# Kernel optimization log

Measured on AMD Instinct MI355X. Metric: run time of the kernel, lower is better.

The kernel has to match this reference:

```python
import jax, jax.numpy as jnp
import numpy as np

D, P, MC = 512, 256, 128   # state dim, obs dim, control dim
H, M, T = 32, 64, 1024     # num filters, Hankel/filter length, horizon
GAMMA = 0.9


def setup_inputs() -> dict:
    rng = np.random.default_rng(0)
    # Stable dynamics: scale spectral radius to 0.95
    A = rng.standard_normal((D, D)).astype(np.float32)
    A *= np.float32(0.95 / np.max(np.abs(np.linalg.eigvals(A))))
    B = (rng.standard_normal((D, MC)) / np.sqrt(D)).astype(np.float32)
    C = (rng.standard_normal((P, D)) / np.sqrt(D)).astype(np.float32)
    # SPD cost matrices
    Q_obs = np.eye(P, dtype=np.float32)
    R = (0.1 * np.eye(MC)).astype(np.float32)
    # LQR-like feedback gain (small, applied to y_obs as in the source)
    K = (0.02 * rng.standard_normal((MC, P))).astype(np.float32)
    # Spectral filters from Hankel matrix: Z_ij = gamma^(i+j+2) * 2/((i+j+2)^3-(i+j+2))
    idx = np.arange(M)
    ij = idx[:, None] + idx[None, :] + 2
    Z = (GAMMA ** ij) * 2.0 / (ij ** 3 - ij)
    w, V = np.linalg.eigh(Z)
    sigma = np.abs(w[-H:])
    phi = V[:, -H:]
    sigma_phi = (sigma ** 0.25)[:, None] * phi.T        # [H, M]
    sigma_phi_M = sigma_phi.astype(np.float32)
    # sum over the inner l-loop of sigma_phi_m (the source sums contributions over l)
    s_m = sigma_phi.sum(axis=1).astype(np.float32)       # [H]
    # Learned controller tensor M_il -> [m_control, H, h, p]
    M_tensor = (0.01 * rng.standard_normal((MC, H, H, P))).astype(np.float32)
    x0 = rng.standard_normal(D).astype(np.float32)
    return {
        "A": jnp.asarray(A), "B": jnp.asarray(B), "C": jnp.asarray(C),
        "Q_obs": jnp.asarray(Q_obs), "R": jnp.asarray(R), "K": jnp.asarray(K),
        "M_tensor": jnp.asarray(M_tensor),
        "sigma_phi_M": jnp.asarray(sigma_phi_M), "s_m": jnp.asarray(s_m),
        "x0": jnp.asarray(x0),
    }


def reference(A, B, C, Q_obs, R, K, M_tensor, sigma_phi_M, s_m, x0):
    h, m = sigma_phi_M.shape          # filters, history window
    mc = B.shape[1]
    p = C.shape[0]

    # CAB[i] = C @ A^i @ B for i = 0..h  (Markov parameters for y_nat)
    def pow_step(Ap, _):
        return Ap @ A, C @ (Ap @ B)
    _, CAB = jax.lax.scan(pow_step, jnp.eye(A.shape[0], dtype=A.dtype), None, length=h + 1)  # [h+1, p, mc]

    # Pre-contract M_tensor with the inner filter weights (sum over j/l):
    # u_pert[c] = sum_{i,k,p'} M2[c,i,p'] * sigma_phi_M[i,k] * y_nat_{t-k}[p']
    M2 = jnp.einsum('cijq,j->ciq', M_tensor, s_m)  # [mc, h, p]

    def step(carry, _):
        x, u_buf, y_buf = carry            # x:[d], u_buf:[h+1,mc] newest-first, y_buf:[m,p] newest-first
        y_obs = C @ x                      # [p]
        # natural observation: strip effect of past controls
        y_nat = y_obs - jnp.einsum('ipc,ic->p', CAB, u_buf)
        y_buf = jnp.concatenate([y_nat[None, :], y_buf[:-1]], axis=0)
        # spectral projection of y_nat history, then contract with learned tensor
        y_proj = sigma_phi_M @ y_buf       # [h, p]
        u_pert = jnp.einsum('ciq,iq->c', M2, y_proj)  # [mc]
        u = -(K @ y_obs) + u_pert
        cost = y_obs @ (Q_obs @ y_obs) + u @ (R @ u)
        u_buf = jnp.concatenate([u[None, :], u_buf[:-1]], axis=0)
        x = A @ x + B @ u
        return (x, u_buf, y_buf), cost

    init = (x0,
            jnp.zeros((h + 1, mc), dtype=x0.dtype),
            jnp.zeros((m, p), dtype=x0.dtype))
    _, costs = jax.lax.scan(step, init, None, length=T)
    return costs  # [T] per-step losses
```

## Files before the change

kernel.cpp:

```cpp
#include <hip/hip_runtime.h>

#define TPB 256
#define MAXJ 48

#define SC_N 128
#define YD0 128
#define YU0 144
#define WD0 151
#define WU0 159
#define DT0 166
#define XP0 182
#define XR0 214
#define U0 230
#define NWG 238
#define NGRP 8
#define GCH 30

__device__ __forceinline__ void cst(float* p, float v) {
  __hip_atomic_store(p, v, __ATOMIC_RELAXED, __HIP_MEMORY_SCOPE_AGENT);
}
__device__ __forceinline__ void cstu(unsigned* p, unsigned v) {
  __hip_atomic_store(p, v, __ATOMIC_RELAXED, __HIP_MEMORY_SCOPE_AGENT);
}
__device__ __forceinline__ unsigned cldu(const unsigned* p) {
  return __hip_atomic_load(p, __ATOMIC_RELAXED, __HIP_MEMORY_SCOPE_AGENT);
}
__device__ __forceinline__ float cld(const float* p) {
  return __hip_atomic_load(p, __ATOMIC_RELAXED, __HIP_MEMORY_SCOPE_AGENT);
}
__device__ __forceinline__ float2 cld2(const float* p) {
  unsigned long long u = __hip_atomic_load(
      reinterpret_cast<const unsigned long long*>(p), __ATOMIC_RELAXED,
      __HIP_MEMORY_SCOPE_AGENT);
  float2 v;
  __builtin_memcpy(&v, &u, 8);
  return v;
}

__device__ __forceinline__ void grid_barrier(unsigned* __restrict__ arr,
                                             unsigned* __restrict__ grp,
                                             int bid, int tid, unsigned phase) {
  asm volatile("s_waitcnt vmcnt(0)" ::: "memory");
  __syncthreads();
  if (tid == 0) cstu(arr + (bid << 5), phase);
  if (bid < NGRP) {
    const int lo = bid * GCH;
    const int n = (NWG - lo < GCH) ? (NWG - lo) : GCH;
    if (tid < n) {
      while (cldu(arr + ((lo + tid) << 5)) < phase) __builtin_amdgcn_s_sleep(1);
    }
    __syncthreads();
    if (tid == 0) cstu(grp + (bid << 5), phase);
  }
  if (tid < NGRP) {
    while (cldu(grp + (tid << 5)) < phase) __builtin_amdgcn_s_sleep(1);
  }
  __atomic_signal_fence(__ATOMIC_SEQ_CST);
  __syncthreads();
}

__device__ void gemm_tile(const float* __restrict__ X, const float* __restrict__ Y,
                          float* __restrict__ Z, int M, int N, int Kd,
                          int mtile, int ntile) {
  __shared__ float Xs[16][65];
  __shared__ float Ys[16][65];
  const int tx = threadIdx.x & 15;
  const int ty = threadIdx.x >> 4;
  const int mbase = mtile * 64;
  const int nbase = ntile * 64;
  float acc[4][4] = {};
  for (int k0 = 0; k0 < Kd; k0 += 16) {
#pragma unroll
    for (int r = 0; r < 4; ++r) {
      int idx = threadIdx.x + 256 * r;
      int mm = idx >> 4, kk = idx & 15;
      int gm = mbase + mm, gk = k0 + kk;
      Xs[kk][mm] = (gm < M && gk < Kd) ? X[(size_t)gm * Kd + gk] : 0.f;
      int nn = idx & 63, k2 = idx >> 6;
      int gn = nbase + nn, gk2 = k0 + k2;
      Ys[k2][nn] = (gk2 < Kd && gn < N) ? Y[(size_t)gk2 * N + gn] : 0.f;
    }
    __syncthreads();
#pragma unroll
    for (int kk = 0; kk < 16; ++kk) {
      float xv[4], yv[4];
#pragma unroll
      for (int a = 0; a < 4; ++a) xv[a] = Xs[kk][ty * 4 + a];
#pragma unroll
      for (int b = 0; b < 4; ++b) yv[b] = Ys[kk][tx * 4 + b];
#pragma unroll
      for (int a = 0; a < 4; ++a)
#pragma unroll
        for (int b = 0; b < 4; ++b) acc[a][b] += xv[a] * yv[b];
    }
    __syncthreads();
  }
#pragma unroll
  for (int a = 0; a < 4; ++a) {
    int gm = mbase + ty * 4 + a;
    if (gm < M) {
#pragma unroll
      for (int b = 0; b < 4; ++b) {
        int gn = nbase + tx * 4 + b;
        if (gn < N) Z[(size_t)gm * N + gn] = acc[a][b];
      }
    }
  }
}

struct JobBatch {
  int n;
  int start[MAXJ + 1];
  int xsel[MAXJ], xoff[MAXJ], ysel[MAXJ], yoff[MAXJ], zoff[MAXJ];
  int M[MAXJ], N[MAXJ], K[MAXJ];
};

__global__ __launch_bounds__(256) void multi_gemm(JobBatch jb,
    const float* __restrict__ A, const float* __restrict__ Bm,
    const float* __restrict__ C, const float* __restrict__ Km,
    float* __restrict__ ws) {
  int b = blockIdx.x;
  int j = 0;
  while (j < jb.n - 1 && b >= jb.start[j + 1]) ++j;
  int rel = b - jb.start[j];
  const float* bases[5] = {ws, A, Bm, C, Km};
  const float* X = bases[jb.xsel[j]] + jb.xoff[j];
  const float* Y = bases[jb.ysel[j]] + jb.yoff[j];
  float* Z = ws + jb.zoff[j];
  int tn = jb.N[j] >> 6;
  gemm_tile(X, Y, Z, jb.M[j], jb.N[j], jb.K[j], rel / tn, rel % tn);
}

__global__ __launch_bounds__(256) void m2_kernel(const float* __restrict__ MT,
    const float* __restrict__ sm, float* __restrict__ M2g) {
  int idx = blockIdx.x * 256 + threadIdx.x;
  if (idx >= 128 * 32 * 256) return;
  int q = idx & 255;
  int ci = idx >> 8;
  const float* base = MT + (size_t)ci * 32 * 256 + q;
  float acc = 0.f;
#pragma unroll
  for (int j = 0; j < 32; ++j) acc += base[j * 256] * sm[j];
  M2g[idx] = acc;
}

__global__ __launch_bounds__(256) void wfir_kernel(const float* __restrict__ M2g,
    const float* __restrict__ Phi, float* __restrict__ W) {
  int idx = blockIdx.x * 256 + threadIdx.x;
  if (idx >= 64 * 32768) return;
  int j = idx >> 15;
  int cq = idx & 32767;
  int c = cq >> 8;
  int q = cq & 255;
  float acc = 0.f;
#pragma unroll
  for (int i = 0; i < 32; ++i)
    acc = fmaf(Phi[(i << 6) | j], M2g[(size_t)(((c << 5) | i) << 8) | q], acc);
  W[idx] = acc;
}

__global__ __launch_bounds__(256) void axpy_acl(const float* __restrict__ A,
    const float* __restrict__ BKC, float* __restrict__ Acl, float* __restrict__ P1) {
  int i = blockIdx.x * 256 + threadIdx.x;
  if (i < 262144) {
    float v = A[i] - BKC[i];
    Acl[i] = v;
    P1[i] = v;
  }
}

__global__ void init_kernel(const float* __restrict__ x0, float* __restrict__ xh,
    float* __restrict__ eh, float* __restrict__ ynh, float* __restrict__ uh0,
    float* __restrict__ dbnd, unsigned* __restrict__ arr,
    unsigned* __restrict__ grp) {
  int i = blockIdx.x * 256 + threadIdx.x;
  int stride = gridDim.x * 256;
  for (int k = i; k < 524288; k += stride) cst(xh + k, 0.f);
  for (int k = i; k < 139264; k += stride) cst(eh + k, 0.f);
  for (int k = i; k < 262144; k += stride) cst(ynh + k, 0.f);
  for (int k = i; k < 8192; k += stride) cst(uh0 + k, 0.f);
  for (int k = i; k < NWG * 32; k += stride) cstu(arr + k, 0u);
  for (int k = i; k < NGRP * 32; k += stride) cstu(grp + k, 0u);
  if (i < 512) cst(dbnd + i, x0[i]);
}

__global__ __launch_bounds__(TPB, 1) void main_kernel(
    const float* __restrict__ B, const float* __restrict__ C,
    const float* __restrict__ x0, const float* __restrict__ Wfir,
    const float* __restrict__ KC, const float* __restrict__ W0C,
    const float* __restrict__ Pp, const float* __restrict__ CAp,
    const float* __restrict__ W0CAp, const float* __restrict__ Rnp,
    const float* __restrict__ AB33p, const float* __restrict__ CAB33p,
    const float* __restrict__ W0CAB33p, const float* __restrict__ A8k,
    float* __restrict__ xh, float* __restrict__ uh0, float* __restrict__ eh,
    float* __restrict__ ynh, float* __restrict__ dbnd,
    unsigned* __restrict__ arr, unsigned* __restrict__ grp) {
  __shared__ float smA[64 * 256];
  __shared__ float smY[8 * 256];
  __shared__ float smV[512];
  __shared__ float smW[8 * 128];
  __shared__ float smVx[8 * 516];
  __shared__ float redsc[4][16];
  const int bid = blockIdx.x;
  const int tid = threadIdx.x;

  if (bid < SC_N) {
    for (int i = tid; i < 16384; i += TPB) {
      int j = i >> 8;
      smA[i] = (j >= 1) ? Wfir[(size_t)j * 32768 + bid * 256 + (i & 255)] : 0.f;
    }
  }
  __syncthreads();

#pragma unroll 1
  for (int ph = 0; ph <= 130; ++ph) {
    const int T = ph * 8;

    if (bid < SC_N) {
      if (ph >= 1 && ph < 129) {
        const int Ty = T - 8;
        const int c = bid;
        for (int i2 = tid; i2 < 1024; i2 += TPB) {
          float2 v = cld2(ynh + (size_t)Ty * 256 + 2 * i2);
          smY[2 * i2] = v.x;
          smY[2 * i2 + 1] = v.y;
        }
        __syncthreads();
        const int q = tid;
        float yreg[8];
#pragma unroll
        for (int s = 0; s < 8; ++s) yreg[s] = smY[s * 256 + q];
        const int wv = tid >> 6;
        const int lane = tid & 63;
#pragma unroll
        for (int kt = 0; kt < 5; ++kt) {
          const int r0 = 1 + 16 * kt;
          float wreg[23];
#pragma unroll
          for (int i = 0; i < 23; ++i) {
            const int j = r0 - 7 + i;
            wreg[i] = (j >= 1 && j <= 63) ? smA[j * 256 + q] : 0.f;
          }
          float acc[16];
#pragma unroll
          for (int a = 0; a < 16; ++a) acc[a] = 0.f;
#pragma unroll
          for (int a = 0; a < 16; ++a)
#pragma unroll
            for (int s = 0; s < 8; ++s) acc[a] += wreg[a + 7 - s] * yreg[s];
#pragma unroll
          for (int a = 0; a < 16; ++a) {
            float v = acc[a];
            v += __shfl_xor(v, 32);
            v += __shfl_xor(v, 16);
            v += __shfl_xor(v, 8);
            v += __shfl_xor(v, 4);
            v += __shfl_xor(v, 2);
            v += __shfl_xor(v, 1);
            if (lane == 0) redsc[wv][a] = v;
          }
          __syncthreads();
          if (tid < 16) {
            const int r = r0 + tid;
            if (r <= 70) {
              float sum = redsc[0][tid] + redsc[1][tid] + redsc[2][tid] + redsc[3][tid];
              atomicAdd(&eh[(size_t)(Ty + r) * 128 + c], sum);
            }
          }
          __syncthreads();
        }
      }
    } else if (bid < YU0) {
      if (ph < 128) {
        const int r = bid - YD0;
        const int s = r >> 1;
        const int half = (r & 1) << 7;
        {
          float2 v = cld2(dbnd + (size_t)ph * 512 + 2 * tid);
          smV[2 * tid] = v.x;
          smV[2 * tid + 1] = v.y;
        }
        __syncthreads();
        const float* Mrow = (s == 0) ? C : (CAp + (size_t)(s - 1) * 131072);
        const int row = half + (tid >> 1);
        const int seg = tid & 1;
        const float4* m4 = (const float4*)(Mrow + (size_t)row * 512 + seg * 256);
        const float4* v4 = (const float4*)(smV + seg * 256);
        float a = 0.f;
#pragma unroll
        for (int it = 0; it < 64; ++it) {
          float4 mm = m4[it], vv = v4[it];
          a += mm.x * vv.x + mm.y * vv.y + mm.z * vv.z + mm.w * vv.w;
        }
        a += __shfl_down(a, 1);
        if (seg == 0) atomicAdd(&ynh[(size_t)(T + s) * 256 + row], a);
        __syncthreads();
      }
    } else if (bid < WD0) {
      if (ph < 128) {
        const int m = bid - YU0;
        for (int i2 = tid; i2 < 512; i2 += TPB) {
          float2 v = cld2(uh0 + (size_t)(64 + T - 33) * 128 + 2 * i2);
          smW[2 * i2] = v.x;
          smW[2 * i2 + 1] = v.y;
        }
        __syncthreads();
        const int row = tid;
        const float4* m4 = (const float4*)(CAB33p + (size_t)m * 32768 + (size_t)row * 128);
        for (int s = m + 1; s < 8; ++s) {
          const float4* u4 = (const float4*)(smW + (s - m - 1) * 128);
          float a = 0.f;
#pragma unroll
          for (int it = 0; it < 32; ++it) {
            float4 mm = m4[it], vv = u4[it];
            a += mm.x * vv.x + mm.y * vv.y + mm.z * vv.z + mm.w * vv.w;
          }
          atomicAdd(&ynh[(size_t)(T + s) * 256 + row], a);
        }
        __syncthreads();
      }
    } else if (bid < WU0) {
      if (ph < 128) {
        const int s = bid - WD0;
        {
          float2 v = cld2(dbnd + (size_t)ph * 512 + 2 * tid);
          smV[2 * tid] = v.x;
          smV[2 * tid + 1] = v.y;
        }
        __syncthreads();
        const float* Mrow = (s == 0) ? W0C : (W0CAp + (size_t)(s - 1) * 65536);
        const int row = tid >> 1;
        const int seg = tid & 1;
        const float4* m4 = (const float4*)(Mrow + (size_t)row * 512 + seg * 256);
        const float4* v4 = (const float4*)(smV + seg * 256);
        float a = 0.f;
#pragma unroll
        for (int it = 0; it < 64; ++it) {
          float4 mm = m4[it], vv = v4[it];
          a += mm.x * vv.x + mm.y * vv.y + mm.z * vv.z + mm.w * vv.w;
        }
        a += __shfl_down(a, 1);
        if (seg == 0) atomicAdd(&eh[(size_t)(T + s) * 128 + row], a);
        __syncthreads();
      }
    } else if (bid < DT0) {
      if (ph < 128) {
        const int m = bid - WU0;
        for (int i2 = tid; i2 < 512; i2 += TPB) {
          float2 v = cld2(uh0 + (size_t)(64 + T - 33) * 128 + 2 * i2);
          smW[2 * i2] = v.x;
          smW[2 * i2 + 1] = v.y;
        }
        __syncthreads();
        const int row = tid >> 1;
        const int seg = tid & 1;
        const float4* m4 = (const float4*)(W0CAB33p + (size_t)m * 16384 + (size_t)row * 128 + seg * 64);
        for (int s = m + 1; s < 8; ++s) {
          const float4* u4 = (const float4*)(smW + (s - m - 1) * 128 + seg * 64);
          float a = 0.f;
#pragma unroll
          for (int it = 0; it < 16; ++it) {
            float4 mm = m4[it], vv = u4[it];
            a += mm.x * vv.x + mm.y * vv.y + mm.z * vv.z + mm.w * vv.w;
          }
          a += __shfl_down(a, 1);
          if (seg == 0) atomicAdd(&eh[(size_t)(T + s) * 128 + row], a);
        }
        __syncthreads();
      }
    } else if (bid < XP0) {
      if (ph < 127) {
        const int g = bid - DT0;
        {
          float2 v = cld2(dbnd + (size_t)ph * 512 + 2 * tid);
          smV[2 * tid] = v.x;
          smV[2 * tid + 1] = v.y;
        }
        for (int i2 = tid; i2 < 512; i2 += TPB) {
          float2 v = cld2(uh0 + (size_t)(64 + T - 33) * 128 + 2 * i2);
          smW[2 * i2] = v.x;
          smW[2 * i2 + 1] = v.y;
        }
        __syncthreads();
        const int row = g * 32 + (tid >> 3);
        const int l4 = tid & 7;
        float a = 0.f;
        {
          const float4* m4 = (const float4*)(A8k + (size_t)row * 512 + l4 * 64);
          const float4* v4 = (const float4*)(smV + l4 * 64);
#pragma unroll
          for (int it = 0; it < 16; ++it) {
            float4 mm = m4[it], vv = v4[it];
            a += mm.x * vv.x + mm.y * vv.y + mm.z * vv.z + mm.w * vv.w;
          }
        }
#pragma unroll
        for (int m = 0; m < 8; ++m) {
          const float4* m4 = (const float4*)(AB33p + (size_t)m * 65536 + (size_t)row * 128 + l4 * 16);
          const float4* v4 = (const float4*)(smW + (7 - m) * 128 + l4 * 16);
#pragma unroll
          for (int it = 0; it < 4; ++it) {
            float4 mm = m4[it], vv = v4[it];
            a += mm.x * vv.x + mm.y * vv.y + mm.z * vv.z + mm.w * vv.w;
          }
        }
        a += __shfl_down(a, 4);
        a += __shfl_down(a, 2);
        a += __shfl_down(a, 1);
        if (l4 == 0) cst(&dbnd[(size_t)(ph + 1) * 512 + row], a);
        __syncthreads();
      }
    } else if (bid < XR0) {
      if (ph >= 2 && ph < 130) {
        const int Tq = T - 16;
        const int r = bid - XP0;
        const int s = r >> 2;
        const int qtr = (r & 3) << 7;
        {
          const float* src = (ph == 2) ? x0 : (xh + (size_t)(Tq - 1) * 512);
          float2 v = cld2(src + 2 * tid);
          smV[2 * tid] = v.x;
          smV[2 * tid + 1] = v.y;
        }
        __syncthreads();
        const int pslot = (ph == 2) ? s : (s + 1);
        const int row = qtr + (tid >> 1);
        const int seg = tid & 1;
        if (pslot == 0) {
          if (seg == 0) atomicAdd(&xh[(size_t)Tq * 512 + row], smV[row]);
        } else {
          const float4* m4 = (const float4*)(Pp + (size_t)(pslot - 1) * 262144 +
                                             (size_t)row * 512 + seg * 256);
          const float4* v4 = (const float4*)(smV + seg * 256);
          float a = 0.f;
#pragma unroll
          for (int it = 0; it < 64; ++it) {
            float4 mm = m4[it], vv = v4[it];
            a += mm.x * vv.x + mm.y * vv.y + mm.z * vv.z + mm.w * vv.w;
          }
          a += __shfl_down(a, 1);
          if (seg == 0) atomicAdd(&xh[(size_t)(Tq + s) * 512 + row], a);
        }
        __syncthreads();
      }
    } else if (bid < U0) {
      if (ph >= 2 && ph < 130) {
        const int Tq = T - 16;
        const int r = bid - XR0;
        const int i = r >> 1;
        const int half = (r & 1) << 8;
        for (int i2 = tid; i2 < 512; i2 += TPB) {
          int idx = 2 * i2;
          float2 v;
          if (ph == 2 && idx < 128) {
            v.x = 0.f;
            v.y = 0.f;
          } else {
            v = cld2(eh + (size_t)(Tq - 1) * 128 + idx);
          }
          smW[idx] = v.x;
          smW[idx + 1] = v.y;
        }
        __syncthreads();
        const int row = half + tid;
        const float* Rrow = (i == 0) ? (B + (size_t)row * 128)
                                     : (Rnp + (size_t)(i - 1) * 65536 + (size_t)row * 128);
        const float4* m4 = (const float4*)Rrow;
        for (int s = i; s < 8; ++s) {
          const float4* e4 = (const float4*)(smW + (s - i) * 128);
          float a = 0.f;
#pragma unroll
          for (int it = 0; it < 32; ++it) {
            float4 mm = m4[it], vv = e4[it];
            a += mm.x * vv.x + mm.y * vv.y + mm.z * vv.z + mm.w * vv.w;
          }
          atomicAdd(&xh[(size_t)(Tq + s) * 512 + row], a);
        }
        __syncthreads();
      }
    } else {
      if (ph >= 3) {
        const int Tu = T - 24;
        const int g = bid - U0;
        for (int i2 = tid; i2 < 2048; i2 += TPB) {
          int idx = 2 * i2;
          int rr = idx >> 9;
          int cc = idx & 511;
          float2 v = cld2(xh + (size_t)(Tu + rr) * 512 + cc);
          smVx[rr * 516 + cc] = v.x;
          smVx[rr * 516 + cc + 1] = v.y;
        }
        __syncthreads();
        const int o = tid >> 1;
        const int par = tid & 1;
        const int s = o >> 4;
        const int lr = o & 15;
        const int row = g * 16 + lr;
        const float4* m4 = (const float4*)(KC + (size_t)row * 512 + par * 256);
        const float4* v4 = (const float4*)(smVx + s * 516 + par * 256);
        float a = 0.f;
#pragma unroll
        for (int it = 0; it < 64; ++it) {
          float4 mm = m4[it], vv = v4[it];
          a += mm.x * vv.x + mm.y * vv.y + mm.z * vv.z + mm.w * vv.w;
        }
        a += __shfl_down(a, 1);
        if (par == 0) {
          float u = cld(&eh[(size_t)(Tu + s) * 128 + row]) - a;
          cst(&uh0[(size_t)(64 + Tu + s) * 128 + row], u);
        }
        __syncthreads();
      }
    }

    grid_barrier(arr, grp, bid, tid, (unsigned)(ph + 1));
  }
}

__global__ __launch_bounds__(256) void cost_kernel(const float* __restrict__ C,
    const float* __restrict__ Q, const float* __restrict__ R,
    const float* __restrict__ xh, const float* __restrict__ uh0,
    float* __restrict__ out) {
  __shared__ float xs[512];
  __shared__ float ys[256];
  __shared__ float us[128];
  __shared__ float redw[4];
  const int t = blockIdx.x;
  const int tid = threadIdx.x;
  {
    float2 v = cld2(xh + (size_t)t * 512 + 2 * tid);
    xs[2 * tid] = v.x;
    xs[2 * tid + 1] = v.y;
  }
  if (tid < 64) {
    float2 v = cld2(uh0 + (size_t)(64 + t) * 128 + 2 * tid);
    us[2 * tid] = v.x;
    us[2 * tid + 1] = v.y;
  }
  __syncthreads();
  {
    const float4* m4 = (const float4*)(C + (size_t)tid * 512);
    const float4* v4 = (const float4*)xs;
    float a = 0.f;
    for (int it = 0; it < 128; ++it) {
      float4 mm = m4[it], vv = v4[it];
      a += mm.x * vv.x + mm.y * vv.y + mm.z * vv.z + mm.w * vv.w;
    }
    ys[tid] = a;
  }
  __syncthreads();
  float acc;
  {
    const float* Qr = Q + (size_t)tid * 256;
    float qy = 0.f;
    for (int k = 0; k < 256; ++k) qy = fmaf(Qr[k], ys[k], qy);
    acc = qy * ys[tid];
  }
  if (tid < 128) {
    const float* Rr = R + (size_t)tid * 128;
    float ru = 0.f;
    for (int k = 0; k < 128; ++k) ru = fmaf(Rr[k], us[k], ru);
    acc += ru * us[tid];
  }
  float v = acc;
  v += __shfl_xor(v, 32);
  v += __shfl_xor(v, 16);
  v += __shfl_xor(v, 8);
  v += __shfl_xor(v, 4);
  v += __shfl_xor(v, 2);
  v += __shfl_xor(v, 1);
  if ((tid & 63) == 0) redw[tid >> 6] = v;
  __syncthreads();
  if (tid == 0) out[t] = redw[0] + redw[1] + redw[2] + redw[3];
}

extern "C" void kernel_launch(void* const* d_in, const int* in_sizes, int n_in,
                              void* d_out, int out_size, void* d_ws, size_t ws_size,
                              hipStream_t stream) {
  (void)in_sizes; (void)n_in; (void)out_size; (void)ws_size;
  const float* A = (const float*)d_in[0];
  const float* B = (const float*)d_in[1];
  const float* C = (const float*)d_in[2];
  const float* Q = (const float*)d_in[3];
  const float* R = (const float*)d_in[4];
  const float* Km = (const float*)d_in[5];
  const float* MT = (const float*)d_in[6];
  const float* Phi = (const float*)d_in[7];
  const float* sm = (const float*)d_in[8];
  const float* x0 = (const float*)d_in[9];

  float* ws = (float*)d_ws;
  const int oWfir = 0;
  const int oKC = 2097152;
  const int oW0C = 2162688;
  const int oAcl = 2228224;
  const int oP = 2490368;
  const int oCA = 4587520;
  const int oW0CA = 5505024;
  const int oRn = 5963776;
  const int oApB = 6422528;
  const int oAB33 = 6946816;
  const int oCAB33 = 7471104;
  const int oW0CAB33 = 7700480;
  const int oA2 = 7815168;
  const int oA4 = 8077312;
  const int oA8 = 8339456;
  const int oA16 = 8601600;
  const int oA32 = 8863744;
  const int oM2 = 9125888;
  const int oBKC = oM2;
  const int oxh = 10174464;
  const int ouh0 = 10698752;
  const int oeh = 10838016;
  const int oynh = 10977280;
  const int odbnd = 11239424;
  const int oarr = 11306496;
  const int ogrp = oarr + NWG * 32;

  float* xh = ws + oxh;
  float* uh0 = ws + ouh0;
  float* eh = ws + oeh;
  float* ynh = ws + oynh;
  float* dbnd = ws + odbnd;
  unsigned* arr = (unsigned*)(ws + oarr);
  unsigned* grp = (unsigned*)(ws + ogrp);

  JobBatch jb;
  jb.n = 0;
  jb.start[0] = 0;
  auto J = [&](int xs_, int xo, int ys_, int yo, int zo, int M, int N, int K) {
    int i = jb.n++;
    jb.xsel[i] = xs_; jb.xoff[i] = xo; jb.ysel[i] = ys_; jb.yoff[i] = yo;
    jb.zoff[i] = zo; jb.M[i] = M; jb.N[i] = N; jb.K[i] = K;
    jb.start[i + 1] = jb.start[i] + (M >> 6) * (N >> 6);
  };
  auto L = [&]() {
    multi_gemm<<<dim3(jb.start[jb.n]), dim3(256), 0, stream>>>(jb, A, B, C, Km, ws);
    jb.n = 0;
    jb.start[0] = 0;
  };

  init_kernel<<<dim3(2048), dim3(256), 0, stream>>>(x0, xh, eh, ynh, uh0, dbnd,
                                                    arr, grp);
  m2_kernel<<<dim3(4096), dim3(256), 0, stream>>>(MT, sm, ws + oM2);
  wfir_kernel<<<dim3(8192), dim3(256), 0, stream>>>(ws + oM2, Phi, ws + oWfir);

  J(4, 0, 3, 0, oKC, 128, 512, 256);
  J(1, 0, 1, 0, oA2, 512, 512, 512);
  J(1, 0, 2, 0, oApB, 512, 128, 512);
  J(3, 0, 1, 0, oCA, 256, 512, 512);
  L();
  J(2, 0, 0, oKC, oBKC, 512, 512, 128);
  J(0, oA2, 0, oA2, oA4, 512, 512, 512);
  J(0, oCA, 1, 0, oCA + 131072, 256, 512, 512);
  J(1, 0, 0, oApB, oApB + 65536, 512, 128, 512);
  J(0, oWfir, 3, 0, oW0C, 128, 512, 256);
  L();
  axpy_acl<<<dim3(1024), dim3(256), 0, stream>>>(A, ws + oBKC, ws + oAcl, ws + oP);
  J(0, oA4, 0, oA4, oA8, 512, 512, 512);
  J(0, oP, 0, oP, oP + 262144, 512, 512, 512);
  J(0, oCA, 0, oA2, oCA + 2 * 131072, 256, 512, 512);
  J(0, oCA + 131072, 0, oA2, oCA + 3 * 131072, 256, 512, 512);
  J(0, oW0C, 1, 0, oW0CA, 128, 512, 512);
  J(0, oW0C, 0, oA2, oW0CA + 65536, 128, 512, 512);
  J(0, oA2, 0, oApB, oApB + 2 * 65536, 512, 128, 512);
  J(0, oA2, 0, oApB + 65536, oApB + 3 * 65536, 512, 128, 512);
  L();
  J(0, oA8, 0, oA8, oA16, 512, 512, 512);
  J(0, oP, 0, oP + 262144, oP + 2 * 262144, 512, 512, 512);
  J(0, oP + 262144, 0, oP + 262144, oP + 3 * 262144, 512, 512, 512);
  for (int i = 1; i <= 3; ++i)
    J(0, oCA + (i - 1) * 131072, 0, oA4, oCA + (i + 3) * 131072, 256, 512, 512);
  for (int i = 1; i <= 2; ++i)
    J(0, oW0CA + (i - 1) * 65536, 0, oA2, oW0CA + (i + 1) * 65536, 128, 512, 512);
  for (int k = 1; k <= 4; ++k)
    J(0, oA4, 0, oApB + (k - 1) * 65536, oApB + (k + 3) * 65536, 512, 128, 512);
  J(0, oP, 2, 0, oRn, 512, 128, 512);
  J(0, oP + 262144, 2, 0, oRn + 65536, 512, 128, 512);
  L();
  J(0, oA16, 0, oA16, oA32, 512, 512, 512);
  for (int i = 1; i <= 4; ++i)
    J(0, oP + (i - 1) * 262144, 0, oP + 3 * 262144, oP + (i + 3) * 262144, 512, 512, 512);
  for (int i = 1; i <= 3; ++i)
    J(0, oW0CA + (i - 1) * 65536, 0, oA4, oW0CA + (i + 3) * 65536, 128, 512, 512);
  J(0, oP + 2 * 262144, 2, 0, oRn + 2 * 65536, 512, 128, 512);
  J(0, oP + 3 * 262144, 2, 0, oRn + 3 * 65536, 512, 128, 512);
  L();
  for (int m = 0; m <= 7; ++m)
    J(0, oA32, 0, oApB + m * 65536, oAB33 + m * 65536, 512, 128, 512);
  for (int i = 5; i <= 7; ++i)
    J(0, oP + (i - 1) * 262144, 2, 0, oRn + (i - 1) * 65536, 512, 128, 512);
  L();
  for (int m = 0; m <= 6; ++m)
    J(3, 0, 0, oAB33 + m * 65536, oCAB33 + m * 32768, 256, 128, 512);
  for (int m = 0; m <= 6; ++m)
    J(0, oW0C, 0, oAB33 + m * 65536, oW0CAB33 + m * 16384, 128, 128, 512);
  L();

  main_kernel<<<dim3(NWG), dim3(TPB), 0, stream>>>(
      B, C, x0, ws + oWfir, ws + oKC, ws + oW0C, ws + oP, ws + oCA,
      ws + oW0CA, ws + oRn, ws + oAB33, ws + oCAB33, ws + oW0CAB33,
      ws + oA8, xh, uh0, eh, ynh, dbnd, arr, grp);

  cost_kernel<<<dim3(1024), dim3(256), 0, stream>>>(C, Q, R, xh, uh0,
                                                    (float*)d_out);
}
```

Baseline: 3.371 ms.

## Cache per-block weight rows in registers across all phases of persistent kernel

Restructures the persistent kernel so each block role has its own phase loop, letting it load its constant matrix rows (C·A^s, W0C, KC, projection, etc.) into float4 register arrays once before the loop. Every phase then does its matvec against registers instead of re-reading the same weights from global/L2. The trailing __syncthreads per phase is dropped, and the XP block's access pattern is interleaved to fit the register layout. This costs up to 256 VGPRs per thread (float4 cm[64]) and risks spills or lower occupancy, which matters little with one block per CU.

```diff
diff --git a/kernel.cpp b/kernel.cpp
--- a/kernel.cpp
+++ b/kernel.cpp
@@ -209,16 +209,11 @@
       int j = i >> 8;
       smA[i] = (j >= 1) ? Wfir[(size_t)j * 32768 + bid * 256 + (i & 255)] : 0.f;
     }
-  }
-  __syncthreads();
-
-#pragma unroll 1
-  for (int ph = 0; ph <= 130; ++ph) {
-    const int T = ph * 8;
-
-    if (bid < SC_N) {
+    __syncthreads();
+#pragma unroll 1
+    for (int ph = 0; ph <= 130; ++ph) {
       if (ph >= 1 && ph < 129) {
-        const int Ty = T - 8;
+        const int Ty = ph * 8 - 8;
         const int c = bid;
         for (int i2 = tid; i2 < 1024; i2 += TPB) {
           float2 v = cld2(ynh + (size_t)Ty * 256 + 2 * i2);
@@ -264,113 +259,167 @@
             const int r = r0 + tid;
             if (r <= 70) {
               float sum = redsc[0][tid] + redsc[1][tid] + redsc[2][tid] + redsc[3][tid];
-              atomicAdd(&eh[(size_t)(Ty + r) * 128 + c], sum);
+              atomicAdd(&eh[(size_t)(Ty + r) * 128 + bid], sum);
             }
           }
           __syncthreads();
         }
-      }
-    } else if (bid < YU0) {
+        (void)c;
+      }
+      grid_barrier(arr, grp, bid, tid, (unsigned)(ph + 1));
+    }
+  } else if (bid < YU0) {
+    const int r = bid - YD0;
+    const int s = r >> 1;
+    const int half = (r & 1) << 7;
+    const int row = half + (tid >> 1);
+    const int seg = tid & 1;
+    const float* Mrow = (s == 0) ? C : (CAp + (size_t)(s - 1) * 131072);
+    const float4* m4 = (const float4*)(Mrow + (size_t)row * 512 + seg * 256);
+    float4 cm[64];
+#pragma unroll
+    for (int it = 0; it < 64; ++it) cm[it] = m4[it];
+#pragma unroll 1
+    for (int ph = 0; ph <= 130; ++ph) {
       if (ph < 128) {
-        const int r = bid - YD0;
-        const int s = r >> 1;
-        const int half = (r & 1) << 7;
+        const int T = ph * 8;
         {
           float2 v = cld2(dbnd + (size_t)ph * 512 + 2 * tid);
           smV[2 * tid] = v.x;
           smV[2 * tid + 1] = v.y;
         }
         __syncthreads();
-        const float* Mrow = (s == 0) ? C : (CAp + (size_t)(s - 1) * 131072);
-        const int row = half + (tid >> 1);
-        const int seg = tid & 1;
-        const float4* m4 = (const float4*)(Mrow + (size_t)row * 512 + seg * 256);
         const float4* v4 = (const float4*)(smV + seg * 256);
         float a = 0.f;
 #pragma unroll
         for (int it = 0; it < 64; ++it) {
-          float4 mm = m4[it], vv = v4[it];
+          float4 mm = cm[it], vv = v4[it];
           a += mm.x * vv.x + mm.y * vv.y + mm.z * vv.z + mm.w * vv.w;
         }
         a += __shfl_down(a, 1);
         if (seg == 0) atomicAdd(&ynh[(size_t)(T + s) * 256 + row], a);
-        __syncthreads();
-      }
-    } else if (bid < WD0) {
+      }
+      grid_barrier(arr, grp, bid, tid, (unsigned)(ph + 1));
+    }
+  } else if (bid < WD0) {
+    const int m = bid - YU0;
+    const int row = tid;
+    const float4* m4 = (const float4*)(CAB33p + (size_t)m * 32768 + (size_t)row * 128);
+    float4 cm[32];
+#pragma unroll
+    for (int it = 0; it < 32; ++it) cm[it] = m4[it];
+#pragma unroll 1
+    for (int ph = 0; ph <= 130; ++ph) {
       if (ph < 128) {
-        const int m = bid - YU0;
+        const int T = ph * 8;
         for (int i2 = tid; i2 < 512; i2 += TPB) {
           float2 v = cld2(uh0 + (size_t)(64 + T - 33) * 128 + 2 * i2);
           smW[2 * i2] = v.x;
           smW[2 * i2 + 1] = v.y;
         }
         __syncthreads();
-        const int row = tid;
-        const float4* m4 = (const float4*)(CAB33p + (size_t)m * 32768 + (size_t)row * 128);
-        for (int s = m + 1; s < 8; ++s) {
-          const float4* u4 = (const float4*)(smW + (s - m - 1) * 128);
-          float a = 0.f;
-#pragma unroll
-          for (int it = 0; it < 32; ++it) {
-            float4 mm = m4[it], vv = u4[it];
-            a += mm.x * vv.x + mm.y * vv.y + mm.z * vv.z + mm.w * vv.w;
-          }
-          atomicAdd(&ynh[(size_t)(T + s) * 256 + row], a);
-        }
-        __syncthreads();
-      }
-    } else if (bid < WU0) {
+#pragma unroll
+        for (int s = 1; s < 8; ++s) {
+          if (s > m) {
+            const float4* u4 = (const float4*)(smW + (s - m - 1) * 128);
+            float a = 0.f;
+#pragma unroll
+            for (int it = 0; it < 32; ++it) {
+              float4 mm = cm[it], vv = u4[it];
+              a += mm.x * vv.x + mm.y * vv.y + mm.z * vv.z + mm.w * vv.w;
+            }
+            atomicAdd(&ynh[(size_t)(T + s) * 256 + row], a);
+          }
+        }
+      }
+      grid_barrier(arr, grp, bid, tid, (unsigned)(ph + 1));
+    }
+  } else if (bid < WU0) {
+    const int s = bid - WD0;
+    const int row = tid >> 1;
+    const int seg = tid & 1;
+    const float* Mrow = (s == 0) ? W0C : (W0CAp + (size_t)(s - 1) * 65536);
+    const float4* m4 = (const float4*)(Mrow + (size_t)row * 512 + seg * 256);
+    float4 cm[64];
+#pragma unroll
+    for (int it = 0; it < 64; ++it) cm[it] = m4[it];
+#pragma unroll 1
+    for (int ph = 0; ph <= 130; ++ph) {
       if (ph < 128) {
-        const int s = bid - WD0;
+        const int T = ph * 8;
         {
           float2 v = cld2(dbnd + (size_t)ph * 512 + 2 * tid);
           smV[2 * tid] = v.x;
           smV[2 * tid + 1] = v.y;
         }
         __syncthreads();
-        const float* Mrow = (s == 0) ? W0C : (W0CAp + (size_t)(s - 1) * 65536);
-        const int row = tid >> 1;
-        const int seg = tid & 1;
-        const float4* m4 = (const float4*)(Mrow + (size_t)row * 512 + seg * 256);
         const float4* v4 = (const float4*)(smV + seg * 256);
         float a = 0.f;
 #pragma unroll
         for (int it = 0; it < 64; ++it) {
-          float4 mm = m4[it], vv = v4[it];
+          float4 mm = cm[it], vv = v4[it];
           a += mm.x * vv.x + mm.y * vv.y + mm.z * vv.z + mm.w * vv.w;
         }
         a += __shfl_down(a, 1);
         if (seg == 0) atomicAdd(&eh[(size_t)(T + s) * 128 + row], a);
-        __syncthreads();
-      }
-    } else if (bid < DT0) {
+      }
+      grid_barrier(arr, grp, bid, tid, (unsigned)(ph + 1));
+    }
+  } else if (bid < DT0) {
+    const int m = bid - WU0;
+    const int row = tid >> 1;
+    const int seg = tid & 1;
+    const float4* m4 = (const float4*)(W0CAB33p + (size_t)m * 16384 + (size_t)row * 128 + seg * 64);
+    float4 cm[16];
+#pragma unroll
+    for (int it = 0; it < 16; ++it) cm[it] = m4[it];
+#pragma unroll 1
+    for (int ph = 0; ph <= 130; ++ph) {
       if (ph < 128) {
-        const int m = bid - WU0;
+        const int T = ph * 8;
         for (int i2 = tid; i2 < 512; i2 += TPB) {
           float2 v = cld2(uh0 + (size_t)(64 + T - 33) * 128 + 2 * i2);
           smW[2 * i2] = v.x;
           smW[2 * i2 + 1] = v.y;
         }
         __syncthreads();
-        const int row = tid >> 1;
-        const int seg = tid & 1;
-        const float4* m4 = (const float4*)(W0CAB33p + (size_t)m * 16384 + (size_t)row * 128 + seg * 64);
-        for (int s = m + 1; s < 8; ++s) {
-          const float4* u4 = (const float4*)(smW + (s - m - 1) * 128 + seg * 64);
-          float a = 0.f;
-#pragma unroll
-          for (int it = 0; it < 16; ++it) {
-            float4 mm = m4[it], vv = u4[it];
-            a += mm.x * vv.x + mm.y * vv.y + mm.z * vv.z + mm.w * vv.w;
-          }
-          a += __shfl_down(a, 1);
-          if (seg == 0) atomicAdd(&eh[(size_t)(T + s) * 128 + row], a);
-        }
-        __syncthreads();
-      }
-    } else if (bid < XP0) {
+#pragma unroll
+        for (int s = 1; s < 8; ++s) {
+          if (s > m) {
+            const float4* u4 = (const float4*)(smW + (s - m - 1) * 128 + seg * 64);
+            float a = 0.f;
+#pragma unroll
+            for (int it = 0; it < 16; ++it) {
+              float4 mm = cm[it], vv = u4[it];
+              a += mm.x * vv.x + mm.y * vv.y + mm.z * vv.z + mm.w * vv.w;
+            }
+            a += __shfl_down(a, 1);
+            if (seg == 0) atomicAdd(&eh[(size_t)(T + s) * 128 + row], a);
+          }
+        }
+      }
+      grid_barrier(arr, grp, bid, tid, (unsigned)(ph + 1));
+    }
+  } else if (bid < XP0) {
+    const int g = bid - DT0;
+    const int row = g * 32 + (tid >> 3);
+    const int l8 = tid & 7;
+    float4 ca[16], cb[32];
+    {
+      const float4* m4 = (const float4*)(A8k + (size_t)row * 512);
+#pragma unroll
+      for (int it = 0; it < 16; ++it) ca[it] = m4[it * 8 + l8];
+    }
+#pragma unroll
+    for (int m = 0; m < 8; ++m) {
+      const float4* m4 = (const float4*)(AB33p + (size_t)m * 65536 + (size_t)row * 128);
+#pragma unroll
+      for (int it = 0; it < 4; ++it) cb[m * 4 + it] = m4[it * 8 + l8];
+    }
+#pragma unroll 1
+    for (int ph = 0; ph <= 130; ++ph) {
       if (ph < 127) {
-        const int g = bid - DT0;
+        const int T = ph * 8;
         {
           float2 v = cld2(dbnd + (size_t)ph * 512 + 2 * tid);
           smV[2 * tid] = v.x;
@@ -382,40 +431,43 @@
           smW[2 * i2 + 1] = v.y;
         }
         __syncthreads();
-        const int row = g * 32 + (tid >> 3);
-        const int l4 = tid & 7;
+        const float4* v4 = (const float4*)smV;
         float a = 0.f;
-        {
-          const float4* m4 = (const float4*)(A8k + (size_t)row * 512 + l4 * 64);
-          const float4* v4 = (const float4*)(smV + l4 * 64);
-#pragma unroll
-          for (int it = 0; it < 16; ++it) {
-            float4 mm = m4[it], vv = v4[it];
-            a += mm.x * vv.x + mm.y * vv.y + mm.z * vv.z + mm.w * vv.w;
-          }
+#pragma unroll
+        for (int it = 0; it < 16; ++it) {
+          float4 mm = ca[it], vv = v4[it * 8 + l8];
+          a += mm.x * vv.x + mm.y * vv.y + mm.z * vv.z + mm.w * vv.w;
         }
 #pragma unroll
         for (int m = 0; m < 8; ++m) {
-          const float4* m4 = (const float4*)(AB33p + (size_t)m * 65536 + (size_t)row * 128 + l4 * 16);
-          const float4* v4 = (const float4*)(smW + (7 - m) * 128 + l4 * 16);
+          const float4* w4 = (const float4*)(smW + (7 - m) * 128);
 #pragma unroll
           for (int it = 0; it < 4; ++it) {
-            float4 mm = m4[it], vv = v4[it];
+            float4 mm = cb[m * 4 + it], vv = w4[it * 8 + l8];
             a += mm.x * vv.x + mm.y * vv.y + mm.z * vv.z + mm.w * vv.w;
           }
         }
         a += __shfl_down(a, 4);
         a += __shfl_down(a, 2);
         a += __shfl_down(a, 1);
-        if (l4 == 0) cst(&dbnd[(size_t)(ph + 1) * 512 + row], a);
-        __syncthreads();
-      }
-    } else if (bid < XR0) {
+        if (l8 == 0) cst(&dbnd[(size_t)(ph + 1) * 512 + row], a);
+      }
+      grid_barrier(arr, grp, bid, tid, (unsigned)(ph + 1));
+    }
+  } else if (bid < XR0) {
+    const int r = bid - XP0;
+    const int s = r >> 2;
+    const int qtr = (r & 3) << 7;
+    const int row = qtr + (tid >> 1);
+    const int seg = tid & 1;
+    const float4* mp = (const float4*)(Pp + (size_t)s * 262144 + (size_t)row * 512 + seg * 256);
+    float4 cm[64];
+#pragma unroll
+    for (int it = 0; it < 64; ++it) cm[it] = mp[it];
+#pragma unroll 1
+    for (int ph = 0; ph <= 130; ++ph) {
       if (ph >= 2 && ph < 130) {
-        const int Tq = T - 16;
-        const int r = bid - XP0;
-        const int s = r >> 2;
-        const int qtr = (r & 3) << 7;
+        const int Tq = ph * 8 - 16;
         {
           const float* src = (ph == 2) ? x0 : (xh + (size_t)(Tq - 1) * 512);
           float2 v = cld2(src + 2 * tid);
@@ -423,32 +475,51 @@
           smV[2 * tid + 1] = v.y;
         }
         __syncthreads();
-        const int pslot = (ph == 2) ? s : (s + 1);
-        const int row = qtr + (tid >> 1);
-        const int seg = tid & 1;
-        if (pslot == 0) {
-          if (seg == 0) atomicAdd(&xh[(size_t)Tq * 512 + row], smV[row]);
+        if (ph == 2) {
+          if (s == 0) {
+            if (seg == 0) atomicAdd(&xh[(size_t)Tq * 512 + row], smV[row]);
+          } else {
+            const float4* m4 = (const float4*)(Pp + (size_t)(s - 1) * 262144 +
+                                               (size_t)row * 512 + seg * 256);
+            const float4* v4 = (const float4*)(smV + seg * 256);
+            float a = 0.f;
+#pragma unroll
+            for (int it = 0; it < 64; ++it) {
+              float4 mm = m4[it], vv = v4[it];
+              a += mm.x * vv.x + mm.y * vv.y + mm.z * vv.z + mm.w * vv.w;
+            }
+            a += __shfl_down(a, 1);
+            if (seg == 0) atomicAdd(&xh[(size_t)(Tq + s) * 512 + row], a);
+          }
         } else {
-          const float4* m4 = (const float4*)(Pp + (size_t)(pslot - 1) * 262144 +
-                                             (size_t)row * 512 + seg * 256);
           const float4* v4 = (const float4*)(smV + seg * 256);
           float a = 0.f;
 #pragma unroll
           for (int it = 0; it < 64; ++it) {
-            float4 mm = m4[it], vv = v4[it];
+            float4 mm = cm[it], vv = v4[it];
             a += mm.x * vv.x + mm.y * vv.y + mm.z * vv.z + mm.w * vv.w;
           }
           a += __shfl_down(a, 1);
           if (seg == 0) atomicAdd(&xh[(size_t)(Tq + s) * 512 + row], a);
         }
-        __syncthreads();
-      }
-    } else if (bid < U0) {
+      }
+      grid_barrier(arr, grp, bid, tid, (unsigned)(ph + 1));
+    }
+  } else if (bid < U0) {
+    const int r = bid - XR0;
+    const int i = r >> 1;
+    const int half = (r & 1) << 8;
+    const int row = half + tid;
+    const float* Rrow = (i == 0) ? (B + (size_t)row * 128)
+                                 : (Rnp + (size_t)(i - 1) * 65536 + (size_t)row * 128);
+    const float4* m4 = (const float4*)Rrow;
+    float4 cm[32];
+#pragma unroll
+    for (int it = 0; it < 32; ++it) cm[it] = m4[it];
+#pragma unroll 1
+    for (int ph = 0; ph <= 130; ++ph) {
       if (ph >= 2 && ph < 130) {
-        const int Tq = T - 16;
-        const int r = bid - XR0;
-        const int i = r >> 1;
-        const int half = (r & 1) << 8;
+        const int Tq = ph * 8 - 16;
         for (int i2 = tid; i2 < 512; i2 += TPB) {
           int idx = 2 * i2;
           float2 v;
@@ -462,26 +533,37 @@
           smW[idx + 1] = v.y;
         }
         __syncthreads();
-        const int row = half + tid;
-        const float* Rrow = (i == 0) ? (B + (size_t)row * 128)
-                                     : (Rnp + (size_t)(i - 1) * 65536 + (size_t)row * 128);
-        const float4* m4 = (const float4*)Rrow;
-        for (int s = i; s < 8; ++s) {
-          const float4* e4 = (const float4*)(smW + (s - i) * 128);
-          float a = 0.f;
-#pragma unroll
-          for (int it = 0; it < 32; ++it) {
-            float4 mm = m4[it], vv = e4[it];
-            a += mm.x * vv.x + mm.y * vv.y + mm.z * vv.z + mm.w * vv.w;
-          }
-          atomicAdd(&xh[(size_t)(Tq + s) * 512 + row], a);
-        }
-        __syncthreads();
-      }
-    } else {
+#pragma unroll
+        for (int s = 0; s < 8; ++s) {
+          if (s >= i) {
+            const float4* e4 = (const float4*)(smW + (s - i) * 128);
+            float a = 0.f;
+#pragma unroll
+            for (int it = 0; it < 32; ++it) {
+              float4 mm = cm[it], vv = e4[it];
+              a += mm.x * vv.x + mm.y * vv.y + mm.z * vv.z + mm.w * vv.w;
+            }
+            atomicAdd(&xh[(size_t)(Tq + s) * 512 + row], a);
+          }
+        }
+      }
+      grid_barrier(arr, grp, bid, tid, (unsigned)(ph + 1));
+    }
+  } else {
+    const int g = bid - U0;
+    const int o = tid >> 1;
+    const int par = tid & 1;
+    const int s = o >> 4;
+    const int lr = o & 15;
+    const int row = g * 16 + lr;
+    const float4* m4 = (const float4*)(KC + (size_t)row * 512 + par * 256);
+    float4 cm[64];
+#pragma unroll
+    for (int it = 0; it < 64; ++it) cm[it] = m4[it];
+#pragma unroll 1
+    for (int ph = 0; ph <= 130; ++ph) {
       if (ph >= 3) {
-        const int Tu = T - 24;
-        const int g = bid - U0;
+        const int Tu = ph * 8 - 24;
         for (int i2 = tid; i2 < 2048; i2 += TPB) {
           int idx = 2 * i2;
           int rr = idx >> 9;
@@ -491,17 +573,11 @@
           smVx[rr * 516 + cc + 1] = v.y;
         }
         __syncthreads();
-        const int o = tid >> 1;
-        const int par = tid & 1;
-        const int s = o >> 4;
-        const int lr = o & 15;
-        const int row = g * 16 + lr;
-        const float4* m4 = (const float4*)(KC + (size_t)row * 512 + par * 256);
         const float4* v4 = (const float4*)(smVx + s * 516 + par * 256);
         float a = 0.f;
 #pragma unroll
         for (int it = 0; it < 64; ++it) {
-          float4 mm = m4[it], vv = v4[it];
+          float4 mm = cm[it], vv = v4[it];
           a += mm.x * vv.x + mm.y * vv.y + mm.z * vv.z + mm.w * vv.w;
         }
         a += __shfl_down(a, 1);
@@ -509,11 +585,9 @@
           float u = cld(&eh[(size_t)(Tu + s) * 128 + row]) - a;
           cst(&uh0[(size_t)(64 + Tu + s) * 128 + row], u);
         }
-        __syncthreads();
-      }
-    }
-
-    grid_barrier(arr, grp, bid, tid, (unsigned)(ph + 1));
+      }
+      grid_barrier(arr, grp, bid, tid, (unsigned)(ph + 1));
+    }
   }
 }
 
```

Measured after the change: 3.353 ms. No clear change (-0.5%).
